# Kernel optimization log

Measured on AMD Instinct MI355X. Metric: run time of the kernel, lower is better.

Reference implementation:

```python
import jax, jax.numpy as jnp
import numpy as np

N = 50000
HID = 128


def care_layer(h, src, dst, att_w, att_b, n_nodes):
    # att([x_i, x_j]) == x_i @ W[:H] + x_j @ W[H:]  (avoids materializing concat)
    H = h.shape[1]
    wi, wj = att_w[:H], att_w[H:]
    hi = h[dst]                                   # [E, H] gather (x_i = target)
    hj = h[src]                                   # [E, H] gather (x_j = source)
    alpha = jax.nn.sigmoid(hi @ wi + hj @ wj + att_b)  # [E, 1]
    msg = alpha * hj                              # [E, H]
    sums = jax.ops.segment_sum(msg, dst, num_segments=n_nodes)
    cnts = jax.ops.segment_sum(jnp.ones((src.shape[0],), h.dtype), dst, num_segments=n_nodes)
    return sums / jnp.maximum(cnts, 1.0)[:, None]  # scatter-mean; isolated nodes -> 0


def setup_inputs() -> dict:
    key = jax.random.key(0)
    ks = jax.random.split(key, 8)
    in_dim, hid, out_dim = 256, HID, 2
    x = jax.random.normal(ks[0], (N, in_dim), dtype=jnp.float32)
    edge_index = jax.random.randint(ks[1], (2, 1600000), 0, N, dtype=jnp.int64)
    s = lambda k, shp, fan: jax.random.normal(k, shp, jnp.float32) * (1.0 / np.sqrt(fan))
    return {
        "x": x,
        "edge_index": edge_index,
        "enc_w": s(ks[2], (in_dim, hid), in_dim),
        "enc_b": jnp.zeros((hid,), jnp.float32),
        "att1_w": s(ks[3], (2 * hid, 1), 2 * hid),
        "att1_b": jnp.zeros((1,), jnp.float32),
        "att2_w": s(ks[4], (2 * hid, 1), 2 * hid),
        "att2_b": jnp.zeros((1,), jnp.float32),
        "cls_w": s(ks[5], (hid, out_dim), hid),
        "cls_b": jnp.zeros((out_dim,), jnp.float32),
    }


def reference(x, edge_index, enc_w, enc_b, att1_w, att1_b, att2_w, att2_b, cls_w, cls_b):
    src, dst = edge_index[0], edge_index[1]  # PyG: x_j = x[src], aggregate at dst
    n = x.shape[0]
    h = jax.nn.relu(x @ enc_w + enc_b)       # dropout is identity in eval mode
    h = care_layer(h, src, dst, att1_w, att1_b, n)
    h = jax.nn.relu(h)
    h = care_layer(h, src, dst, att2_w, att2_b, n)
    return h @ cls_w + cls_b                 # [N, out_dim]
```

## Files before the change

kernel.cpp:

```cpp
#include <hip/hip_runtime.h>
#include <hip/hip_bf16.h>
#include <hip/hip_fp16.h>
#include <math.h>

#define HID 128
#define INDIM 256
#define CAP 6144
#define NBLK1 256

__global__ void detect_i64_kernel(const int* __restrict__ idx32, int* __restrict__ flag) {
    int l = threadIdx.x;
    int v = idx32[2 * l + 1];
    unsigned long long ball = __ballot(v != 0);
    if (l == 0) flag[0] = (ball == 0ULL) ? 1 : 0;
}

__device__ __forceinline__ int load_src(const int* idx, int is64, int E, int e) {
    return is64 ? idx[2 * e] : idx[e];
}
__device__ __forceinline__ int load_dst(const int* idx, int is64, int E, int e) {
    return is64 ? idx[2 * (E + e)] : idx[E + e];
}

__global__ __launch_bounds__(256) void bucket_scatter_kernel(const int* __restrict__ idx32,
                                                             const int* __restrict__ flag,
                                                             int* __restrict__ bcursor,
                                                             unsigned int* __restrict__ recs,
                                                             int E, int NB) {
    __shared__ int hist[512];
    __shared__ int cur[512];
    int t = threadIdx.x;
    int CH = (E + NBLK1 - 1) / NBLK1;
    int e0 = blockIdx.x * CH;
    int e1 = min(e0 + CH, E);
    for (int i = t; i < NB; i += 256) hist[i] = 0;
    __syncthreads();
    int is64 = flag[0];
    for (int e = e0 + t; e < e1; e += 256) {
        int d = load_dst(idx32, is64, E, e);
        atomicAdd(&hist[d >> 7], 1);
    }
    __syncthreads();
    for (int i = t; i < NB; i += 256)
        cur[i] = atomicAdd(&bcursor[i], hist[i]);
    __syncthreads();
    for (int e = e0 + t; e < e1; e += 256) {
        int s = load_src(idx32, is64, E, e);
        int d = load_dst(idx32, is64, E, e);
        int b = d >> 7;
        int r = atomicAdd(&cur[b], 1);
        recs[(size_t)b * CAP + r] = ((unsigned)d << 16) | (unsigned)s;
    }
}

__global__ void bucket_scan_kernel(const int* __restrict__ bcursor,
                                   int* __restrict__ bbase, int NB) {
    int l = threadIdx.x;
    int i0 = l * 8;
    int v[8];
    #pragma unroll
    for (int k = 0; k < 8; k++) v[k] = (i0 + k < NB) ? bcursor[i0 + k] : 0;
    int s = 0;
    #pragma unroll
    for (int k = 0; k < 8; k++) s += v[k];
    int x = s;
    #pragma unroll
    for (int off = 1; off < 64; off <<= 1) {
        int y = __shfl_up(x, off);
        if (l >= off) x += y;
    }
    int run = x - s;
    #pragma unroll
    for (int k = 0; k < 8; k++) {
        if (i0 + k < NB) bbase[i0 + k] = run;
        run += v[k];
    }
}

__global__ __launch_bounds__(256) void csr_finalize_kernel(const unsigned int* __restrict__ recs,
                                                           const int* __restrict__ bcursor,
                                                           const int* __restrict__ bbase,
                                                           int* __restrict__ rowstart,
                                                           int* __restrict__ csr_src,
                                                           int N, int E) {
    __shared__ int h[128];
    __shared__ int ex[128];
    __shared__ int cu[128];
    int b = blockIdx.x;
    int t = threadIdx.x;
    int cnt = bcursor[b];
    int base = bbase[b];
    if (t < 128) h[t] = 0;
    __syncthreads();
    const unsigned int* r0 = recs + (size_t)b * CAP;
    for (int i = t; i < cnt; i += 256) {
        unsigned int rec = r0[i];
        atomicAdd(&h[(rec >> 16) & 127], 1);
    }
    __syncthreads();
    if (t < 64) {
        int a0 = h[2 * t], a1 = h[2 * t + 1];
        int s = a0 + a1;
        int x = s;
        #pragma unroll
        for (int off = 1; off < 64; off <<= 1) {
            int y = __shfl_up(x, off);
            if (t >= off) x += y;
        }
        ex[2 * t] = x - s;
        ex[2 * t + 1] = x - s + a0;
    }
    __syncthreads();
    int d0 = b * 128;
    if (t < 128) {
        if (d0 + t < N) rowstart[d0 + t] = base + ex[t];
        cu[t] = ex[t];
    }
    if (b == 0 && t == 0) rowstart[N] = E;
    __syncthreads();
    for (int i = t; i < cnt; i += 256) {
        unsigned int rec = r0[i];
        int dl = (rec >> 16) & 127;
        int r = atomicAdd(&cu[dl], 1);
        csr_src[base + r] = (int)(rec & 0xffffu);
    }
}

__global__ __launch_bounds__(256) void encoder_kernel(const float* __restrict__ x,
                                                      const float* __restrict__ W,
                                                      const float* __restrict__ b,
                                                      const float* __restrict__ attw,
                                                      const float* __restrict__ attb,
                                                      __half* __restrict__ h16,
                                                      float* __restrict__ ai,
                                                      float* __restrict__ aj, int N) {
    __shared__ float xs[64][36];
    __shared__ float ws[32][128];
    int t = threadIdx.x;
    int n0 = blockIdx.x * 64;
    int tc = t & 15, tr = t >> 4;
    int c0 = tc * 8, r0 = tr * 4;
    float acc[4][8];
    #pragma unroll
    for (int i = 0; i < 4; i++)
        #pragma unroll
        for (int j = 0; j < 8; j++) acc[i][j] = 0.f;

    int lr = t >> 2, lc = (t & 3) * 8;
    int wr = t >> 3, wc = (t & 7) * 16;

    for (int k0 = 0; k0 < INDIM; k0 += 32) {
        int gr = n0 + lr; if (gr >= N) gr = N - 1;
        const float4* xg = (const float4*)(x + (size_t)gr * INDIM + k0 + lc);
        float4 a0 = xg[0], a1 = xg[1];
        *(float4*)&xs[lr][lc]     = a0;
        *(float4*)&xs[lr][lc + 4] = a1;
        const float4* wg = (const float4*)(W + (size_t)(k0 + wr) * HID + wc);
        float4 b0 = wg[0], b1 = wg[1], b2 = wg[2], b3 = wg[3];
        *(float4*)&ws[wr][wc]      = b0;
        *(float4*)&ws[wr][wc + 4]  = b1;
        *(float4*)&ws[wr][wc + 8]  = b2;
        *(float4*)&ws[wr][wc + 12] = b3;
        __syncthreads();
        #pragma unroll
        for (int kk = 0; kk < 32; ++kk) {
            float xv[4];
            #pragma unroll
            for (int i = 0; i < 4; i++) xv[i] = xs[r0 + i][kk];
            float4 w0 = *(float4*)&ws[kk][c0];
            float4 w1 = *(float4*)&ws[kk][c0 + 4];
            float wv[8] = {w0.x, w0.y, w0.z, w0.w, w1.x, w1.y, w1.z, w1.w};
            #pragma unroll
            for (int i = 0; i < 4; i++)
                #pragma unroll
                for (int j = 0; j < 8; j++)
                    acc[i][j] = fmaf(xv[i], wv[j], acc[i][j]);
        }
        __syncthreads();
    }
    float wiv[8], wjv[8];
    #pragma unroll
    for (int j = 0; j < 8; j++) { wiv[j] = attw[c0 + j]; wjv[j] = attw[HID + c0 + j]; }
    #pragma unroll
    for (int i = 0; i < 4; i++) {
        int gr = n0 + r0 + i;
        float ov[8];
        #pragma unroll
        for (int j = 0; j < 8; j++) {
            float o = acc[i][j] + b[c0 + j];
            ov[j] = o > 0.f ? o : 0.f;
        }
        if (gr < N) {
            union { float4 f; __half2 h[4]; } u;
            #pragma unroll
            for (int j = 0; j < 8; j += 2)
                u.h[j >> 1] = __float22half2_rn(make_float2(ov[j], ov[j + 1]));
            *(float4*)(h16 + (size_t)gr * HID + c0) = u.f;
        }
        float pi = 0.f, pj = 0.f;
        #pragma unroll
        for (int j = 0; j < 8; j++) { pi = fmaf(ov[j], wiv[j], pi); pj = fmaf(ov[j], wjv[j], pj); }
        #pragma unroll
        for (int off = 1; off < 16; off <<= 1) {
            pi += __shfl_xor(pi, off);
            pj += __shfl_xor(pj, off);
        }
        if (tc == 0 && gr < N) { ai[gr] = pi + attb[0]; aj[gr] = pj; }
    }
}

template <int MODE>
__global__ __launch_bounds__(256) void care_kernel(const __half* __restrict__ hh,
                                                   const float* __restrict__ ai,
                                                   const float* __restrict__ aj,
                                                   const int* __restrict__ rowstart,
                                                   const int* __restrict__ csr_src,
                                                   float* __restrict__ out,
                                                   __half* __restrict__ hh_out,
                                                   float* __restrict__ ai2,
                                                   float* __restrict__ aj2, int N,
                                                   const float* __restrict__ attw2,
                                                   const float* __restrict__ attb2,
                                                   const float* __restrict__ clsw,
                                                   const float* __restrict__ clsb) {
    int t = threadIdx.x;
    int lane = t & 63, w = t >> 6;
    int n = blockIdx.x * 4 + w;
    if (n >= N) return;
    int beg = rowstart[n], end = rowstart[n + 1];
    int deg = end - beg;
    float ain = ai[n];
    int g = lane >> 4;
    int r = lane & 15;

    float acc[8];
    #pragma unroll
    for (int k = 0; k < 8; k++) acc[k] = 0.f;

    const float4* hp = (const float4*)hh;
    for (int c0 = beg; c0 < end; c0 += 64) {
        int m = end - c0; if (m > 64) m = 64;
        int li = lane < m ? lane : m - 1;
        int sl = csr_src[c0 + li];
        float ajl = aj[sl];
        float al = 1.0f / (1.0f + __expf(-(ain + ajl)));
        if (lane >= m) al = 0.f;
        int nit = (m + 3) >> 2;
        #pragma unroll 4
        for (int it = 0; it < nit; ++it) {
            int idx = it * 4 + g;
            float a = __shfl(al, idx);
            int s = __shfl(sl, idx);
            float4 hv = hp[(size_t)s * 16 + r];
            union { float4 f; __half2 h[4]; } u; u.f = hv;
            #pragma unroll
            for (int k = 0; k < 4; k++) {
                float2 fv = __half22float2(u.h[k]);
                acc[2 * k + 0] = fmaf(a, fv.x, acc[2 * k + 0]);
                acc[2 * k + 1] = fmaf(a, fv.y, acc[2 * k + 1]);
            }
        }
    }
    #pragma unroll
    for (int k = 0; k < 8; k++) {
        acc[k] += __shfl_xor(acc[k], 16);
        acc[k] += __shfl_xor(acc[k], 32);
    }
    float scale = 1.0f / fmaxf((float)deg, 1.0f);

    if (MODE == 0) {
        float mv[8];
        #pragma unroll
        for (int k = 0; k < 8; k++) {
            float o = acc[k] * scale;
            mv[k] = o > 0.f ? o : 0.f;
        }
        if (g == 0) {
            union { float4 f; __half2 h[4]; } u;
            #pragma unroll
            for (int k = 0; k < 4; k++)
                u.h[k] = __float22half2_rn(make_float2(mv[2 * k], mv[2 * k + 1]));
            ((float4*)hh_out)[(size_t)n * 16 + r] = u.f;
        }
        float pi = 0.f, pj = 0.f;
        #pragma unroll
        for (int k = 0; k < 8; k++) {
            int f = r * 8 + k;
            pi = fmaf(mv[k], attw2[f], pi);
            pj = fmaf(mv[k], attw2[HID + f], pj);
        }
        #pragma unroll
        for (int off = 1; off < 16; off <<= 1) {
            pi += __shfl_xor(pi, off);
            pj += __shfl_xor(pj, off);
        }
        if (lane == 0) { ai2[n] = pi + attb2[0]; aj2[n] = pj; }
    } else {
        float p0 = 0.f, p1 = 0.f;
        #pragma unroll
        for (int k = 0; k < 8; k++) {
            float m = acc[k] * scale;
            int f = r * 8 + k;
            p0 = fmaf(m, clsw[f * 2 + 0], p0);
            p1 = fmaf(m, clsw[f * 2 + 1], p1);
        }
        #pragma unroll
        for (int off = 8; off >= 1; off >>= 1) {
            p0 += __shfl_xor(p0, off);
            p1 += __shfl_xor(p1, off);
        }
        if (lane == 0) {
            out[(size_t)n * 2 + 0] = p0 + clsb[0];
            out[(size_t)n * 2 + 1] = p1 + clsb[1];
        }
    }
}

extern "C" void kernel_launch(void* const* d_in, const int* in_sizes, int n_in,
                              void* d_out, int out_size, void* d_ws, size_t ws_size,
                              hipStream_t stream) {
    const float* x      = (const float*)d_in[0];
    const int*   idx32  = (const int*)d_in[1];
    const float* enc_w  = (const float*)d_in[2];
    const float* enc_b  = (const float*)d_in[3];
    const float* att1_w = (const float*)d_in[4];
    const float* att1_b = (const float*)d_in[5];
    const float* att2_w = (const float*)d_in[6];
    const float* att2_b = (const float*)d_in[7];
    const float* cls_w  = (const float*)d_in[8];
    const float* cls_b  = (const float*)d_in[9];
    float* out = (float*)d_out;

    int N = in_sizes[0] / INDIM;
    int E = in_sizes[1] / 2;
    int NB = (N + 127) >> 7;

    char* p = (char*)d_ws;
    __half* h16a = (__half*)p; p += (size_t)N * HID * 2;
    __half* h16b = (__half*)p; p += (size_t)N * HID * 2;
    int* csr_src  = (int*)p; p += (size_t)E * 4;
    unsigned int* recs = (unsigned int*)p; p += (size_t)NB * CAP * 4;
    float* ai   = (float*)p; p += (size_t)N * 4;
    float* aj   = (float*)p; p += (size_t)N * 4;
    float* ai2  = (float*)p; p += (size_t)N * 4;
    float* aj2  = (float*)p; p += (size_t)N * 4;
    int* rowstart = (int*)p; p += (size_t)(N + 1) * 4;
    int* bcursor  = (int*)p; p += (size_t)NB * 4;
    int* bbase    = (int*)p; p += (size_t)NB * 4;
    int* flag     = (int*)p; p += 64;

    hipMemsetAsync(bcursor, 0, (size_t)NB * 4, stream);
    detect_i64_kernel<<<1, 64, 0, stream>>>(idx32, flag);
    bucket_scatter_kernel<<<NBLK1, 256, 0, stream>>>(idx32, flag, bcursor, recs, E, NB);
    bucket_scan_kernel<<<1, 64, 0, stream>>>(bcursor, bbase, NB);
    csr_finalize_kernel<<<NB, 256, 0, stream>>>(recs, bcursor, bbase, rowstart,
                                                csr_src, N, E);

    encoder_kernel<<<(N + 63) / 64, 256, 0, stream>>>(x, enc_w, enc_b, att1_w, att1_b,
                                                      h16a, ai, aj, N);

    care_kernel<0><<<(N + 3) / 4, 256, 0, stream>>>(h16a, ai, aj, rowstart, csr_src,
                                                    nullptr, h16b, ai2, aj2, N,
                                                    att2_w, att2_b, nullptr, nullptr);
    care_kernel<1><<<(N + 3) / 4, 256, 0, stream>>>(h16b, ai2, aj2, rowstart, csr_src,
                                                    out, nullptr, nullptr, nullptr, N,
                                                    nullptr, nullptr, cls_w, cls_b);
}
```

Baseline: 303.5 us.

## Use packed fp16 dot2 in encoder GEMM and double bucket block count

```diff
diff --git a/kernel.cpp b/kernel.cpp
--- a/kernel.cpp
+++ b/kernel.cpp
@@ -6,7 +6,20 @@
 #define HID 128
 #define INDIM 256
 #define CAP 6144
-#define NBLK1 256
+#define NBLK1 512
+
+typedef _Float16 h2v __attribute__((ext_vector_type(2)));
+
+#ifndef __has_builtin
+#define __has_builtin(x) 0
+#endif
+#if __has_builtin(__builtin_amdgcn_fdot2)
+#define FDOT2(a, b, c) __builtin_amdgcn_fdot2((a), (b), (c), false)
+#else
+__device__ __forceinline__ float FDOT2(h2v a, h2v b, float c) {
+    return fmaf((float)a[0], (float)b[0], fmaf((float)a[1], (float)b[1], c));
+}
+#endif
 
 __global__ void detect_i64_kernel(const int* __restrict__ idx32, int* __restrict__ flag) {
     int l = threadIdx.x;
@@ -134,8 +147,8 @@
                                                       __half* __restrict__ h16,
                                                       float* __restrict__ ai,
                                                       float* __restrict__ aj, int N) {
-    __shared__ float xs[64][36];
-    __shared__ float ws[32][128];
+    __shared__ h2v xsp[16][68];
+    __shared__ h2v wspT[16][132];
     int t = threadIdx.x;
     int n0 = blockIdx.x * 64;
     int tc = t & 15, tr = t >> 4;
@@ -146,35 +159,50 @@
         #pragma unroll
         for (int j = 0; j < 8; j++) acc[i][j] = 0.f;
 
-    int lr = t >> 2, lc = (t & 3) * 8;
-    int wr = t >> 3, wc = (t & 7) * 16;
+    int lr = t >> 2, lc4 = (t & 3) * 8;
+    int wcg = t & 15, wk2 = t >> 4;
 
     for (int k0 = 0; k0 < INDIM; k0 += 32) {
         int gr = n0 + lr; if (gr >= N) gr = N - 1;
-        const float4* xg = (const float4*)(x + (size_t)gr * INDIM + k0 + lc);
+        const float4* xg = (const float4*)(x + (size_t)gr * INDIM + k0 + lc4);
         float4 a0 = xg[0], a1 = xg[1];
-        *(float4*)&xs[lr][lc]     = a0;
-        *(float4*)&xs[lr][lc + 4] = a1;
-        const float4* wg = (const float4*)(W + (size_t)(k0 + wr) * HID + wc);
-        float4 b0 = wg[0], b1 = wg[1], b2 = wg[2], b3 = wg[3];
-        *(float4*)&ws[wr][wc]      = b0;
-        *(float4*)&ws[wr][wc + 4]  = b1;
-        *(float4*)&ws[wr][wc + 8]  = b2;
-        *(float4*)&ws[wr][wc + 12] = b3;
+        int kb = lc4 >> 1;
+        { h2v p; p[0] = (_Float16)a0.x; p[1] = (_Float16)a0.y; xsp[kb + 0][lr] = p; }
+        { h2v p; p[0] = (_Float16)a0.z; p[1] = (_Float16)a0.w; xsp[kb + 1][lr] = p; }
+        { h2v p; p[0] = (_Float16)a1.x; p[1] = (_Float16)a1.y; xsp[kb + 2][lr] = p; }
+        { h2v p; p[0] = (_Float16)a1.z; p[1] = (_Float16)a1.w; xsp[kb + 3][lr] = p; }
+        {
+            const float4* w0 = (const float4*)(W + (size_t)(k0 + 2 * wk2) * HID + wcg * 8);
+            const float4* w1 = (const float4*)(W + (size_t)(k0 + 2 * wk2 + 1) * HID + wcg * 8);
+            float4 r0a = w0[0], r0b = w0[1];
+            float4 r1a = w1[0], r1b = w1[1];
+            union { float4 f; h2v h[4]; } ua, ub;
+            ua.h[0][0] = (_Float16)r0a.x; ua.h[0][1] = (_Float16)r1a.x;
+            ua.h[1][0] = (_Float16)r0a.y; ua.h[1][1] = (_Float16)r1a.y;
+            ua.h[2][0] = (_Float16)r0a.z; ua.h[2][1] = (_Float16)r1a.z;
+            ua.h[3][0] = (_Float16)r0a.w; ua.h[3][1] = (_Float16)r1a.w;
+            ub.h[0][0] = (_Float16)r0b.x; ub.h[0][1] = (_Float16)r1b.x;
+            ub.h[1][0] = (_Float16)r0b.y; ub.h[1][1] = (_Float16)r1b.y;
+            ub.h[2][0] = (_Float16)r0b.z; ub.h[2][1] = (_Float16)r1b.z;
+            ub.h[3][0] = (_Float16)r0b.w; ub.h[3][1] = (_Float16)r1b.w;
+            *(float4*)&wspT[wcg][wk2 * 8]     = ua.f;
+            *(float4*)&wspT[wcg][wk2 * 8 + 4] = ub.f;
+        }
         __syncthreads();
         #pragma unroll
-        for (int kk = 0; kk < 32; ++kk) {
-            float xv[4];
+        for (int kk2 = 0; kk2 < 16; ++kk2) {
+            union { float4 f; h2v h[4]; } ux, uw0, uw1;
+            ux.f  = *(const float4*)&xsp[kk2][r0];
+            uw0.f = *(const float4*)&wspT[tc][kk2 * 8];
+            uw1.f = *(const float4*)&wspT[tc][kk2 * 8 + 4];
             #pragma unroll
-            for (int i = 0; i < 4; i++) xv[i] = xs[r0 + i][kk];
-            float4 w0 = *(float4*)&ws[kk][c0];
-            float4 w1 = *(float4*)&ws[kk][c0 + 4];
-            float wv[8] = {w0.x, w0.y, w0.z, w0.w, w1.x, w1.y, w1.z, w1.w};
-            #pragma unroll
-            for (int i = 0; i < 4; i++)
+            for (int i = 0; i < 4; i++) {
                 #pragma unroll
-                for (int j = 0; j < 8; j++)
-                    acc[i][j] = fmaf(xv[i], wv[j], acc[i][j]);
+                for (int j = 0; j < 4; j++) {
+                    acc[i][j]     = FDOT2(ux.h[i], uw0.h[j], acc[i][j]);
+                    acc[i][j + 4] = FDOT2(ux.h[i], uw1.h[j], acc[i][j + 4]);
+                }
+            }
         }
         __syncthreads();
     }
```

Result: faster. 293.5 us (-3.3%).
